# Kernel tuning notes

Measured on AMD Instinct MI355X. Metric: run time of the kernel, lower is better.

## Reference

```python
import jax, jax.numpy as jnp
import numpy as np

N_NODES = 50000
N_EDGES = 1600000
D = 128
LEAKY_SLOPE = 0.01  # torch nn.LeakyReLU default


def setup_inputs() -> dict:
    key = jax.random.key(0)
    ks = jax.random.split(key, 7)
    entity_embed = jax.random.normal(ks[0], (N_NODES, D), dtype=jnp.float32)
    W1 = jax.random.normal(ks[1], (D, D), dtype=jnp.float32) * 0.05
    b1 = jax.random.normal(ks[2], (D,), dtype=jnp.float32) * 0.05
    W2 = jax.random.normal(ks[3], (D, D), dtype=jnp.float32) * 0.05
    b2 = jax.random.normal(ks[4], (D,), dtype=jnp.float32) * 0.05
    src = jax.random.randint(ks[5], (N_EDGES,), 0, N_NODES, dtype=jnp.int32)
    dst = jax.random.randint(ks[6], (N_EDGES,), 0, N_NODES, dtype=jnp.int32)
    return {"entity_embed": entity_embed, "W1": W1, "b1": b1,
            "W2": W2, "b2": b2, "src": src, "dst": dst}


def reference(entity_embed, W1, b1, W2, b2, src, dst):
    # DGL update_all(copy_u('node','side'), sum('side','H')):
    # H[v] = sum over edges (u -> v) of entity_embed[u]
    n = entity_embed.shape[0]
    H = jax.ops.segment_sum(entity_embed[src], dst, num_segments=n)  # [N, D]
    # neighbors branch: LeakyReLU(W_1 @ H)
    neighbors = jax.nn.leaky_relu(H @ W1.T + b1, negative_slope=LEAKY_SLOPE)
    # interactions branch: LeakyReLU(W_2 @ (node * H))
    interactions = jax.nn.leaky_relu((entity_embed * H) @ W2.T + b2,
                                     negative_slope=LEAKY_SLOPE)
    # dropout is identity at inference
    return neighbors + interactions
```

## Files before the change

### kernel.cpp

```cpp
#include <hip/hip_runtime.h>

#define NN 50000
#define DD 128
#define SLOPE 0.01f
#define NB 782
#define BCAP 2304
#define NSB 49
#define SBW 1024
#define SCAP 34816
#define ECH1 4096
#define RSL 2048
#define RS 17
#define OVCAP 8192
#define HP 136

using bf16x8 = __attribute__((ext_vector_type(8))) short;
using f32x4  = __attribute__((ext_vector_type(4))) float;

__device__ inline float bflo(unsigned int w) { return __uint_as_float(w << 16); }
__device__ inline float bfhi(unsigned int w) { return __uint_as_float(w & 0xffff0000u); }
__device__ inline float sbf(short s) {
    return __uint_as_float(((unsigned int)(unsigned short)s) << 16);
}
__device__ inline unsigned int rnebf(float f) {
    unsigned int u = __float_as_uint(f);
    return (u + 0x7fffu + ((u >> 16) & 1u)) >> 16;
}
__device__ inline unsigned int pack2(float lo, float hi) {
    return rnebf(lo) | (rnebf(hi) << 16);
}
__device__ inline void addrow(float* acc, uint4 r) {
    acc[0] += bflo(r.x); acc[1] += bfhi(r.x);
    acc[2] += bflo(r.y); acc[3] += bfhi(r.y);
    acc[4] += bflo(r.z); acc[5] += bfhi(r.z);
    acc[6] += bflo(r.w); acc[7] += bfhi(r.w);
}

__device__ inline void convert_item(
    const float* __restrict__ E, const float* __restrict__ W1,
    const float* __restrict__ W2, unsigned short* __restrict__ Ebf,
    unsigned short* __restrict__ W1b, unsigned short* __restrict__ W2b, int t)
{
    const int NE8 = NN * DD / 8;
    const int NW8 = DD * DD / 8;
    const float* s; unsigned short* d; int idx;
    if (t < NE8)                { s = E;  d = Ebf; idx = t; }
    else if (t < NE8 + NW8)     { s = W1; d = W1b; idx = t - NE8; }
    else if (t < NE8 + 2 * NW8) { s = W2; d = W2b; idx = t - NE8 - NW8; }
    else return;
    float4 a = ((const float4*)s)[(size_t)idx * 2];
    float4 b = ((const float4*)s)[(size_t)idx * 2 + 1];
    uint4 o;
    o.x = pack2(a.x, a.y); o.y = pack2(a.z, a.w);
    o.z = pack2(b.x, b.y); o.w = pack2(b.z, b.w);
    ((uint4*)d)[idx] = o;
}

__global__ __launch_bounds__(512) void scatter_convert(
    const float* __restrict__ E, const float* __restrict__ W1,
    const float* __restrict__ W2, const int* __restrict__ src,
    const int* __restrict__ dst, unsigned short* __restrict__ Ebf,
    unsigned short* __restrict__ W1b, unsigned short* __restrict__ W2b,
    int* __restrict__ gtail1, unsigned int* __restrict__ stag1,
    int* __restrict__ ovf_cnt, int2* __restrict__ ovf,
    int n_edges, int nch1)
{
    const int tid = threadIdx.x;
    if (blockIdx.x >= nch1) {
        convert_item(E, W1, W2, Ebf, W1b, W2b,
                     (blockIdx.x - nch1) * 512 + tid);
        return;
    }

    __shared__ int cnt49[NSB];
    const int e0 = blockIdx.x * ECH1;
    int vv[8], uu[8];

    if (tid < NSB) cnt49[tid] = 0;
    __syncthreads();
    #pragma unroll
    for (int k = 0; k < 8; ++k) {
        int idx = e0 + tid + k * 512;
        if (idx < n_edges) {
            vv[k] = dst[idx]; uu[k] = src[idx];
            atomicAdd(&cnt49[vv[k] >> 10], 1);
        } else vv[k] = -1;
    }
    __syncthreads();
    if (tid < NSB) {
        int c = cnt49[tid];
        cnt49[tid] = c ? atomicAdd(&gtail1[tid], c) : 0;
    }
    __syncthreads();
    #pragma unroll
    for (int k = 0; k < 8; ++k) {
        if (vv[k] < 0) continue;
        int sb = vv[k] >> 10;
        int p = atomicAdd(&cnt49[sb], 1);
        if (p < SCAP) {
            stag1[(size_t)sb * SCAP + p] =
                (unsigned int)uu[k] | ((unsigned int)(vv[k] & 1023) << 16);
        } else {
            int oi = atomicAdd(ovf_cnt, 1);
            if (oi < OVCAP) ovf[oi] = make_int2(uu[k], vv[k]);
        }
    }
}

__global__ __launch_bounds__(256) void rebin(
    const int* __restrict__ gtail1, const unsigned int* __restrict__ stag1,
    int* __restrict__ gtail, unsigned int* __restrict__ stag,
    int* __restrict__ ovf_cnt, int2* __restrict__ ovf)
{
    const int sb = blockIdx.x / RS, sl = blockIdx.x % RS;
    const int tid = threadIdx.x;
    int len = gtail1[sb]; len = len < SCAP ? len : SCAP;
    const int i0 = sl * RSL;
    const int i1 = min(i0 + RSL, len);

    __shared__ int cnt16[16], pos16[16];
    if (tid < 16) cnt16[tid] = 0;
    __syncthreads();

    unsigned int r[8];
    const unsigned int* seg = stag1 + (size_t)sb * SCAP;
    #pragma unroll
    for (int k = 0; k < 8; ++k) {
        int idx = i0 + tid + k * 256;
        if (idx < i1) {
            r[k] = seg[idx];
            atomicAdd(&cnt16[(r[k] >> 22) & 15], 1);
        } else r[k] = 0xffffffffu;
    }
    __syncthreads();
    if (tid < 16) {
        int c = cnt16[tid];
        int bb = sb * 16 + tid;
        pos16[tid] = (c && bb < NB) ? atomicAdd(&gtail[bb], c) : 0;
    }
    __syncthreads();
    #pragma unroll
    for (int k = 0; k < 8; ++k) {
        if (r[k] == 0xffffffffu) continue;
        int j = (r[k] >> 22) & 15;
        int p = atomicAdd(&pos16[j], 1);
        int bb = sb * 16 + j;
        if (p < BCAP) {
            stag[(size_t)bb * BCAP + p] = r[k] & 0x3fffffu;
        } else {
            int oi = atomicAdd(ovf_cnt, 1);
            if (oi < OVCAP)
                ovf[oi] = make_int2((int)(r[k] & 0xffffu),
                                    sb * SBW + (int)((r[k] >> 16) & 1023));
        }
    }
}

__global__ __launch_bounds__(256, 4) void bucket_fused(
    const unsigned short* __restrict__ Ebf, const int* __restrict__ gtail,
    const unsigned int* __restrict__ stag, const int* __restrict__ ovf_cnt,
    const int2* __restrict__ ovf,
    const unsigned short* __restrict__ W1b, const unsigned short* __restrict__ W2b,
    const float* __restrict__ b1, const float* __restrict__ b2,
    float* __restrict__ out)
{
    __shared__ unsigned short sorted[BCAP];
    __shared__ unsigned short Hs[64][HP];
    __shared__ int cnt[64], off[65], pos[64];
    __shared__ int s_novf;

    const int b = blockIdx.x;
    const int tid = threadIdx.x;
    int len = gtail[b]; len = len < BCAP ? len : BCAP;
    const unsigned int* seg = stag + (size_t)b * BCAP;

    if (tid == 0) { int t = *ovf_cnt; s_novf = t < OVCAP ? t : OVCAP; }
    if (tid < 64) cnt[tid] = 0;
    __syncthreads();
    for (int i = tid; i < len; i += 256)
        atomicAdd(&cnt[(seg[i] >> 16) & 63], 1);
    __syncthreads();
    if (tid < 64) {
        int cv = cnt[tid];
        int incl = cv;
        #pragma unroll
        for (int d = 1; d < 64; d <<= 1) {
            int t2 = __shfl_up(incl, d);
            if (tid >= d) incl += t2;
        }
        off[tid] = incl - cv;
        pos[tid] = incl - cv;
        if (tid == 63) off[64] = incl;
    }
    __syncthreads();
    for (int i = tid; i < len; i += 256) {
        unsigned int r = seg[i];
        int p = atomicAdd(&pos[(r >> 16) & 63], 1);
        sorted[p] = (unsigned short)(r & 0xffffu);
    }
    __syncthreads();
    const int novf = s_novf;

    const int g = tid >> 4;
    const int c = tid & 15;
    const uint4* E4 = (const uint4*)Ebf;
    for (int p4 = 0; p4 < 4; ++p4) {
        int nl = p4 * 16 + g;
        int v = b * 64 + nl;
        if (v >= NN) continue;
        float acc[8] = {};
        int i = off[nl], e1 = off[nl + 1];
        uint4 r[16];
        for (; i + 16 <= e1; i += 16) {
            #pragma unroll
            for (int k = 0; k < 16; ++k)
                r[k] = E4[(size_t)sorted[i + k] * 16 + c];
            __builtin_amdgcn_sched_barrier(0);
            #pragma unroll
            for (int k = 0; k < 16; ++k) addrow(acc, r[k]);
        }
        for (; i + 4 <= e1; i += 4) {
            #pragma unroll
            for (int k = 0; k < 4; ++k)
                r[k] = E4[(size_t)sorted[i + k] * 16 + c];
            __builtin_amdgcn_sched_barrier(0);
            #pragma unroll
            for (int k = 0; k < 4; ++k) addrow(acc, r[k]);
        }
        for (; i < e1; ++i) addrow(acc, E4[(size_t)sorted[i] * 16 + c]);

        if (novf > 0) {
            for (int k = 0; k < novf; ++k) {
                int2 e = ovf[k];
                if (e.y == v) addrow(acc, E4[(size_t)e.x * 16 + c]);
            }
        }
        uint4 o;
        o.x = pack2(acc[0], acc[1]); o.y = pack2(acc[2], acc[3]);
        o.z = pack2(acc[4], acc[5]); o.w = pack2(acc[6], acc[7]);
        *(uint4*)&Hs[nl][c * 8] = o;
    }
    __syncthreads();

    const int wave = tid >> 6;
    const int lane = tid & 63;
    const int v0 = b * 64 + wave * 16;
    if (v0 >= NN) return;
    const int m = lane & 15;
    const int quad = lane >> 4;

    bf16x8 aH[4], aE[4];
    const unsigned short* hrow = &Hs[wave * 16 + m][quad * 8];
    const unsigned short* erow = Ebf + (size_t)(v0 + m) * DD + quad * 8;
    #pragma unroll
    for (int ks = 0; ks < 4; ++ks) {
        bf16x8 h8 = *(const bf16x8*)(hrow + ks * 32);
        bf16x8 e8 = *(const bf16x8*)(erow + ks * 32);
        aH[ks] = h8;
        bf16x8 eh;
        #pragma unroll
        for (int j = 0; j < 8; ++j)
            eh[j] = (short)rnebf(sbf(h8[j]) * sbf(e8[j]));
        aE[ks] = eh;
    }

    #pragma unroll
    for (int jt = 0; jt < 8; ++jt) {
        const int j0 = jt * 16;
        const unsigned short* w1r = W1b + (size_t)(j0 + m) * DD + quad * 8;
        const unsigned short* w2r = W2b + (size_t)(j0 + m) * DD + quad * 8;
        f32x4 acc1 = {0.f, 0.f, 0.f, 0.f}, acc2 = {0.f, 0.f, 0.f, 0.f};
        #pragma unroll
        for (int ks = 0; ks < 4; ++ks) {
            bf16x8 bw1 = *(const bf16x8*)(w1r + ks * 32);
            bf16x8 bw2 = *(const bf16x8*)(w2r + ks * 32);
            acc1 = __builtin_amdgcn_mfma_f32_16x16x32_bf16(aH[ks], bw1, acc1, 0, 0, 0);
            acc2 = __builtin_amdgcn_mfma_f32_16x16x32_bf16(aE[ks], bw2, acc2, 0, 0, 0);
        }
        const float bb1 = b1[j0 + m], bb2 = b2[j0 + m];
        #pragma unroll
        for (int i = 0; i < 4; ++i) {
            int row = v0 + quad * 4 + i;
            if (row < NN) {
                float x1 = acc1[i] + bb1; x1 = x1 > 0.f ? x1 : SLOPE * x1;
                float x2 = acc2[i] + bb2; x2 = x2 > 0.f ? x2 : SLOPE * x2;
                out[(size_t)row * DD + j0 + m] = x1 + x2;
            }
        }
    }
}

__global__ __launch_bounds__(256) void scatter_add(
    const float* __restrict__ E, const int* __restrict__ src,
    const int* __restrict__ dst, float* __restrict__ H, int n_edges)
{
    int t = blockIdx.x * 256 + threadIdx.x;
    int e = t >> 5;
    if (e >= n_edges) return;
    int c = t & 31;
    float4 a = ((const float4*)E)[(size_t)src[e] * 32 + c];
    float* hp = H + (size_t)dst[e] * DD + c * 4;
    atomicAdd(hp + 0, a.x); atomicAdd(hp + 1, a.y);
    atomicAdd(hp + 2, a.z); atomicAdd(hp + 3, a.w);
}

__global__ __launch_bounds__(256) void fused_mlp(
    const float* __restrict__ E, const float* __restrict__ H,
    const float* __restrict__ W1, const float* __restrict__ b1,
    const float* __restrict__ W2, const float* __restrict__ b2,
    float* __restrict__ out)
{
    __shared__ float Hsf[32][DD];
    __shared__ float EHs[32][DD];
    __shared__ float W1s[DD][20];
    __shared__ float W2s[DD][20];
    const int tid = threadIdx.x;
    const int v0 = blockIdx.x * 32;
    const int nvalid = min(32, NN - v0);
    for (int i = 0; i < 4; ++i) {
        int f = tid + 256 * i;
        int n = f >> 5, c = f & 31;
        float4 h = make_float4(0.f, 0.f, 0.f, 0.f);
        float4 eh = h;
        if (n < nvalid) {
            h = ((const float4*)H)[(size_t)(v0 + n) * 32 + c];
            float4 e4 = ((const float4*)E)[(size_t)(v0 + n) * 32 + c];
            eh = make_float4(e4.x * h.x, e4.y * h.y, e4.z * h.z, e4.w * h.w);
        }
        *((float4*)&Hsf[n][c * 4]) = h;
        *((float4*)&EHs[n][c * 4]) = eh;
    }
    const int jg = tid & 63;
    const int n0 = (tid >> 6) * 8;
    float acc1a[8] = {}, acc1b[8] = {}, acc2a[8] = {}, acc2b[8] = {};
    for (int t8 = 0; t8 < 8; ++t8) {
        const int k0 = t8 * 16;
        __syncthreads();
        for (int i = 0; i < 8; ++i) {
            int f = tid + 256 * i;
            int j = f >> 4, kk = f & 15;
            W1s[j][kk] = W1[j * DD + k0 + kk];
            W2s[j][kk] = W2[j * DD + k0 + kk];
        }
        __syncthreads();
        for (int c = 0; c < 4; ++c) {
            float4 w1a = *((const float4*)&W1s[jg][c * 4]);
            float4 w1b = *((const float4*)&W1s[jg + 64][c * 4]);
            float4 w2a = *((const float4*)&W2s[jg][c * 4]);
            float4 w2b = *((const float4*)&W2s[jg + 64][c * 4]);
            const int kk = k0 + c * 4;
            for (int n = 0; n < 8; ++n) {
                float4 h = *((const float4*)&Hsf[n0 + n][kk]);
                float4 eh = *((const float4*)&EHs[n0 + n][kk]);
                acc1a[n] += h.x * w1a.x + h.y * w1a.y + h.z * w1a.z + h.w * w1a.w;
                acc1b[n] += h.x * w1b.x + h.y * w1b.y + h.z * w1b.z + h.w * w1b.w;
                acc2a[n] += eh.x * w2a.x + eh.y * w2a.y + eh.z * w2a.z + eh.w * w2a.w;
                acc2b[n] += eh.x * w2b.x + eh.y * w2b.y + eh.z * w2b.z + eh.w * w2b.w;
            }
        }
    }
    const float b1a = b1[jg], b1b = b1[jg + 64];
    const float b2a = b2[jg], b2b = b2[jg + 64];
    for (int n = 0; n < 8; ++n) {
        if (n0 + n < nvalid) {
            const int v = v0 + n0 + n;
            float x1 = acc1a[n] + b1a; x1 = x1 > 0.f ? x1 : SLOPE * x1;
            float x2 = acc2a[n] + b2a; x2 = x2 > 0.f ? x2 : SLOPE * x2;
            out[(size_t)v * DD + jg] = x1 + x2;
            float y1 = acc1b[n] + b1b; y1 = y1 > 0.f ? y1 : SLOPE * y1;
            float y2 = acc2b[n] + b2b; y2 = y2 > 0.f ? y2 : SLOPE * y2;
            out[(size_t)v * DD + jg + 64] = y1 + y2;
        }
    }
}

extern "C" void kernel_launch(void* const* d_in, const int* in_sizes, int n_in,
                              void* d_out, int out_size, void* d_ws, size_t ws_size,
                              hipStream_t stream)
{
    const float* E  = (const float*)d_in[0];
    const float* W1 = (const float*)d_in[1];
    const float* b1 = (const float*)d_in[2];
    const float* W2 = (const float*)d_in[3];
    const float* b2 = (const float*)d_in[4];
    const int* src  = (const int*)d_in[5];
    const int* dst  = (const int*)d_in[6];
    float* out = (float*)d_out;
    const int n_edges = in_sizes[5];

    char* ws = (char*)d_ws;
    auto al = [](size_t x) { return (x + 255) & ~(size_t)255; };

    const int nch1 = (n_edges + ECH1 - 1) / ECH1;

    const size_t ctr_ints  = NSB + 1 + NB;
    const size_t off_ovf   = al(ctr_ints * 4);
    const size_t off_stag1 = al(off_ovf + (size_t)OVCAP * 8);
    const size_t off_stag  = al(off_stag1 + (size_t)NSB * SCAP * 4);
    const size_t off_Ebf   = al(off_stag + (size_t)NB * BCAP * 4);
    const size_t off_W1b   = al(off_Ebf + (size_t)NN * DD * 2);
    const size_t off_W2b   = al(off_W1b + (size_t)DD * DD * 2);
    const size_t need_bf   = off_W2b + (size_t)DD * DD * 2;

    if (ws_size >= need_bf) {
        int*  gtail1  = (int*)ws;
        int*  ovf_cnt = gtail1 + NSB;
        int*  gtail   = gtail1 + NSB + 1;
        int2* ovf     = (int2*)(ws + off_ovf);
        unsigned int*   stag1 = (unsigned int*)(ws + off_stag1);
        unsigned int*   stag  = (unsigned int*)(ws + off_stag);
        unsigned short* Ebf   = (unsigned short*)(ws + off_Ebf);
        unsigned short* W1b   = (unsigned short*)(ws + off_W1b);
        unsigned short* W2b   = (unsigned short*)(ws + off_W2b);

        const int NCV  = NN * DD / 8 + 2 * (DD * DD / 8);
        const int ncvb = (NCV + 511) / 512;

        hipMemsetAsync(ws, 0, ctr_ints * 4, stream);
        scatter_convert<<<nch1 + ncvb, 512, 0, stream>>>(
            E, W1, W2, src, dst, Ebf, W1b, W2b,
            gtail1, stag1, ovf_cnt, ovf, n_edges, nch1);
        rebin<<<NSB * RS, 256, 0, stream>>>(
            gtail1, stag1, gtail, stag, ovf_cnt, ovf);
        bucket_fused<<<NB, 256, 0, stream>>>(
            Ebf, gtail, stag, ovf_cnt, ovf, W1b, W2b, b1, b2, out);
        return;
    }

    const size_t hbytes = (size_t)NN * DD * sizeof(float);
    float* H = (ws_size >= hbytes) ? (float*)ws : out;
    hipMemsetAsync(H, 0, hbytes, stream);
    scatter_add<<<((n_edges * 32) + 255) / 256, 256, 0, stream>>>(
        E, src, dst, H, n_edges);
    fused_mlp<<<(NN + 31) / 32, 256, 0, stream>>>(E, H, W1, b1, W2, b2, out);
}
```

Measured before the change: 195.8 us.

## Split bucket gather and GEMM into separate kernels with half-row blocks

Replaces the fused gather+MLP kernel with two kernels: a gather kernel launched with two blocks per bucket, each accumulating half of the feature columns into an fp32 H buffer in workspace, and a separate MFMA GEMM kernel that reads H, converts to bf16 and applies both linear branches. The gather also sorts edges by (node, source-row high bits) to improve locality of embedding reads, and the fused fallback's unroll depth is reduced from 16 to 8. The split doubles gather parallelism and removes the LDS-limited fusion, but adds a full fp32 H write and read round-trip plus an extra launch.

New measurement: 193.5 us. No clear change (-1.2%).

```diff
diff --git a/kernel.cpp b/kernel.cpp
--- a/kernel.cpp
+++ b/kernel.cpp
@@ -156,6 +156,165 @@
     }
 }
 
+__global__ __launch_bounds__(256, 4) void bucket_gather(
+    const unsigned short* __restrict__ Ebf, const int* __restrict__ gtail,
+    const unsigned int* __restrict__ stag, const int* __restrict__ ovf_cnt,
+    const int2* __restrict__ ovf, float* __restrict__ Hf)
+{
+    __shared__ unsigned short sorted[BCAP];
+    __shared__ int cnt1k[1024];
+    __shared__ int bstart[1025];
+    __shared__ int wsum[4];
+    __shared__ int s_novf;
+
+    const int b = blockIdx.x >> 1;
+    const int h = blockIdx.x & 1;
+    const int tid = threadIdx.x;
+    int len = gtail[b]; len = len < BCAP ? len : BCAP;
+    const unsigned int* seg = stag + (size_t)b * BCAP;
+
+    if (tid == 0) { int t = *ovf_cnt; s_novf = t < OVCAP ? t : OVCAP; }
+    #pragma unroll
+    for (int j = 0; j < 4; ++j) cnt1k[tid * 4 + j] = 0;
+    __syncthreads();
+    for (int i = tid; i < len; i += 256) {
+        unsigned int r = seg[i];
+        int key = (int)(((r >> 16) & 63) << 4) | (int)((r & 0xffffu) >> 12);
+        atomicAdd(&cnt1k[key], 1);
+    }
+    __syncthreads();
+    {
+        const int lane = tid & 63, w = tid >> 6;
+        int c[4], loc[4]; int s = 0;
+        #pragma unroll
+        for (int j = 0; j < 4; ++j) {
+            c[j] = cnt1k[tid * 4 + j]; loc[j] = s; s += c[j];
+        }
+        int incl = s;
+        #pragma unroll
+        for (int d = 1; d < 64; d <<= 1) {
+            int t2 = __shfl_up(incl, d);
+            if (lane >= d) incl += t2;
+        }
+        if (lane == 63) wsum[w] = incl;
+        __syncthreads();
+        int wbase = 0;
+        for (int w2 = 0; w2 < w; ++w2) wbase += wsum[w2];
+        int base = wbase + incl - s;
+        #pragma unroll
+        for (int j = 0; j < 4; ++j) {
+            bstart[tid * 4 + j] = base + loc[j];
+            cnt1k[tid * 4 + j]  = base + loc[j];
+        }
+        if (tid == 255) bstart[1024] = base + s;
+    }
+    __syncthreads();
+    for (int i = tid; i < len; i += 256) {
+        unsigned int r = seg[i];
+        int key = (int)(((r >> 16) & 63) << 4) | (int)((r & 0xffffu) >> 12);
+        int p = atomicAdd(&cnt1k[key], 1);
+        sorted[p] = (unsigned short)(r & 0xffffu);
+    }
+    __syncthreads();
+    const int novf = s_novf;
+
+    const int g = tid >> 3;
+    const int c = tid & 7;
+    const uint4* E4 = (const uint4*)Ebf;
+    for (int p2 = 0; p2 < 2; ++p2) {
+        int nl = p2 * 32 + g;
+        int v = b * 64 + nl;
+        if (v >= NN) continue;
+        float acc[8] = {};
+        int i = bstart[nl << 4], e1 = bstart[(nl + 1) << 4];
+        uint4 r[8];
+        for (; i + 8 <= e1; i += 8) {
+            #pragma unroll
+            for (int k = 0; k < 8; ++k)
+                r[k] = E4[(size_t)sorted[i + k] * 16 + h * 8 + c];
+            __builtin_amdgcn_sched_barrier(0);
+            #pragma unroll
+            for (int k = 0; k < 8; ++k) addrow(acc, r[k]);
+        }
+        for (; i + 2 <= e1; i += 2) {
+            uint4 r0 = E4[(size_t)sorted[i]     * 16 + h * 8 + c];
+            uint4 r1 = E4[(size_t)sorted[i + 1] * 16 + h * 8 + c];
+            addrow(acc, r0); addrow(acc, r1);
+        }
+        if (i < e1) addrow(acc, E4[(size_t)sorted[i] * 16 + h * 8 + c]);
+
+        if (novf > 0) {
+            for (int k = 0; k < novf; ++k) {
+                int2 e = ovf[k];
+                if (e.y == v) addrow(acc, E4[(size_t)e.x * 16 + h * 8 + c]);
+            }
+        }
+        float* o = Hf + (size_t)v * DD + h * 64 + c * 8;
+        *(float4*)o       = make_float4(acc[0], acc[1], acc[2], acc[3]);
+        *(float4*)(o + 4) = make_float4(acc[4], acc[5], acc[6], acc[7]);
+    }
+}
+
+__global__ __launch_bounds__(256) void bucket_gemm(
+    const float* __restrict__ Hf, const unsigned short* __restrict__ Ebf,
+    const unsigned short* __restrict__ W1b, const unsigned short* __restrict__ W2b,
+    const float* __restrict__ b1, const float* __restrict__ b2,
+    float* __restrict__ out)
+{
+    const int b = blockIdx.x;
+    const int tid = threadIdx.x;
+    const int wave = tid >> 6;
+    const int lane = tid & 63;
+    const int v0 = b * 64 + wave * 16;
+    if (v0 >= NN) return;
+    const int m = lane & 15;
+    const int quad = lane >> 4;
+
+    bf16x8 aH[4], aE[4];
+    const float* hrow = Hf + (size_t)(v0 + m) * DD + quad * 8;
+    const unsigned short* erow = Ebf + (size_t)(v0 + m) * DD + quad * 8;
+    #pragma unroll
+    for (int ks = 0; ks < 4; ++ks) {
+        float4 f0 = *(const float4*)(hrow + ks * 32);
+        float4 f1 = *(const float4*)(hrow + ks * 32 + 4);
+        bf16x8 e8 = *(const bf16x8*)(erow + ks * 32);
+        bf16x8 h8, eh;
+        h8[0] = (short)rnebf(f0.x); h8[1] = (short)rnebf(f0.y);
+        h8[2] = (short)rnebf(f0.z); h8[3] = (short)rnebf(f0.w);
+        h8[4] = (short)rnebf(f1.x); h8[5] = (short)rnebf(f1.y);
+        h8[6] = (short)rnebf(f1.z); h8[7] = (short)rnebf(f1.w);
+        #pragma unroll
+        for (int j = 0; j < 8; ++j)
+            eh[j] = (short)rnebf(sbf(h8[j]) * sbf(e8[j]));
+        aH[ks] = h8; aE[ks] = eh;
+    }
+
+    #pragma unroll
+    for (int jt = 0; jt < 8; ++jt) {
+        const int j0 = jt * 16;
+        const unsigned short* w1r = W1b + (size_t)(j0 + m) * DD + quad * 8;
+        const unsigned short* w2r = W2b + (size_t)(j0 + m) * DD + quad * 8;
+        f32x4 acc1 = {0.f, 0.f, 0.f, 0.f}, acc2 = {0.f, 0.f, 0.f, 0.f};
+        #pragma unroll
+        for (int ks = 0; ks < 4; ++ks) {
+            bf16x8 bw1 = *(const bf16x8*)(w1r + ks * 32);
+            bf16x8 bw2 = *(const bf16x8*)(w2r + ks * 32);
+            acc1 = __builtin_amdgcn_mfma_f32_16x16x32_bf16(aH[ks], bw1, acc1, 0, 0, 0);
+            acc2 = __builtin_amdgcn_mfma_f32_16x16x32_bf16(aE[ks], bw2, acc2, 0, 0, 0);
+        }
+        const float bb1 = b1[j0 + m], bb2 = b2[j0 + m];
+        #pragma unroll
+        for (int i = 0; i < 4; ++i) {
+            int row = v0 + quad * 4 + i;
+            if (row < NN) {
+                float x1 = acc1[i] + bb1; x1 = x1 > 0.f ? x1 : SLOPE * x1;
+                float x2 = acc2[i] + bb2; x2 = x2 > 0.f ? x2 : SLOPE * x2;
+                out[(size_t)row * DD + j0 + m] = x1 + x2;
+            }
+        }
+    }
+}
+
 __global__ __launch_bounds__(256, 4) void bucket_fused(
     const unsigned short* __restrict__ Ebf, const int* __restrict__ gtail,
     const unsigned int* __restrict__ stag, const int* __restrict__ ovf_cnt,
@@ -210,25 +369,21 @@
         if (v >= NN) continue;
         float acc[8] = {};
         int i = off[nl], e1 = off[nl + 1];
-        uint4 r[16];
-        for (; i + 16 <= e1; i += 16) {
+        uint4 r[8];
+        for (; i + 8 <= e1; i += 8) {
             #pragma unroll
-            for (int k = 0; k < 16; ++k)
+            for (int k = 0; k < 8; ++k)
                 r[k] = E4[(size_t)sorted[i + k] * 16 + c];
             __builtin_amdgcn_sched_barrier(0);
             #pragma unroll
-            for (int k = 0; k < 16; ++k) addrow(acc, r[k]);
-        }
-        for (; i + 4 <= e1; i += 4) {
-            #pragma unroll
-            for (int k = 0; k < 4; ++k)
-                r[k] = E4[(size_t)sorted[i + k] * 16 + c];
-            __builtin_amdgcn_sched_barrier(0);
-            #pragma unroll
-            for (int k = 0; k < 4; ++k) addrow(acc, r[k]);
-        }
-        for (; i < e1; ++i) addrow(acc, E4[(size_t)sorted[i] * 16 + c]);
-
+            for (int k = 0; k < 8; ++k) addrow(acc, r[k]);
+        }
+        for (; i + 2 <= e1; i += 2) {
+            uint4 r0 = E4[(size_t)sorted[i]     * 16 + c];
+            uint4 r1 = E4[(size_t)sorted[i + 1] * 16 + c];
+            addrow(acc, r0); addrow(acc, r1);
+        }
+        if (i < e1) addrow(acc, E4[(size_t)sorted[i] * 16 + c]);
         if (novf > 0) {
             for (int k = 0; k < novf; ++k) {
                 int2 e = ovf[k];
@@ -263,7 +418,6 @@
             eh[j] = (short)rnebf(sbf(h8[j]) * sbf(e8[j]));
         aE[ks] = eh;
     }
-
     #pragma unroll
     for (int jt = 0; jt < 8; ++jt) {
         const int j0 = jt * 16;
@@ -401,6 +555,8 @@
     const size_t off_W1b   = al(off_Ebf + (size_t)NN * DD * 2);
     const size_t off_W2b   = al(off_W1b + (size_t)DD * DD * 2);
     const size_t need_bf   = off_W2b + (size_t)DD * DD * 2;
+    const size_t off_Hf    = al(need_bf);
+    const size_t need_split = off_Hf + (size_t)NN * DD * 4;
 
     if (ws_size >= need_bf) {
         int*  gtail1  = (int*)ws;
@@ -422,8 +578,17 @@
             gtail1, stag1, ovf_cnt, ovf, n_edges, nch1);
         rebin<<<NSB * RS, 256, 0, stream>>>(
             gtail1, stag1, gtail, stag, ovf_cnt, ovf);
-        bucket_fused<<<NB, 256, 0, stream>>>(
-            Ebf, gtail, stag, ovf_cnt, ovf, W1b, W2b, b1, b2, out);
+
+        if (ws_size >= need_split) {
+            float* Hf = (float*)(ws + off_Hf);
+            bucket_gather<<<NB * 2, 256, 0, stream>>>(
+                Ebf, gtail, stag, ovf_cnt, ovf, Hf);
+            bucket_gemm<<<NB, 256, 0, stream>>>(
+                Hf, Ebf, W1b, W2b, b1, b2, out);
+        } else {
+            bucket_fused<<<NB, 256, 0, stream>>>(
+                Ebf, gtail, stag, ovf_cnt, ovf, W1b, W2b, b1, b2, out);
+        }
         return;
     }
 
```
